# Performance work log

Measured on AMD Instinct MI355X. Metric: run time of the kernel, lower is better.

Reference implementation:

```python
import jax, jax.numpy as jnp
import numpy as np

B, T, D = 4, 2048, 1024
NF = 512
NB = 4
FREQ_SCALE = 0.1


def _w(k, shape, scale):
    return jax.random.normal(k, shape, jnp.float32) * scale


def setup_inputs() -> dict:
    key = jax.random.key(0)
    ks = jax.random.split(key, 16)
    d = D ** -0.5
    inp = {}
    inp['x'] = jax.random.normal(ks[0], (B, T, D), jnp.float32)
    inp['norm_g'] = jnp.ones((D,), jnp.float32)
    inp['norm_b'] = jnp.zeros((D,), jnp.float32)
    inp['Wconcept'] = _w(ks[1], (D, D), d); inp['bconcept'] = jnp.zeros((D,), jnp.float32)
    inp['Wcg'] = _w(ks[2], (D, D), d); inp['bcg'] = jnp.zeros((D,), jnp.float32)
    inp['Wfg'] = _w(ks[3], (NF, D), d); inp['bfg'] = jnp.zeros((NF,), jnp.float32)
    inp['Wtg'] = _w(ks[4], (1, D), d); inp['btg'] = jnp.zeros((1,), jnp.float32)
    inp['Wband'] = _w(ks[5], (NB, D), d); inp['bband'] = jnp.zeros((NB,), jnp.float32)
    inp['Wsp'] = _w(ks[6], (2 * NF, D), d)  # to_spectral, no bias
    inp['freq_importance'] = jnp.ones((NF,), jnp.float32)
    inp['log_decay'] = (jnp.linspace(-3.0, -0.001, NF) + _w(ks[7], (NF,), 0.1)).astype(jnp.float32)
    inp['frequencies'] = ((jnp.arange(NF, dtype=jnp.float32) / NF * 2.0 - 1.0) * 0.2)
    inp['dt'] = jnp.ones((NF,), jnp.float32) * 0.5
    inp['Wgate'] = _w(ks[8], (D, D), d); inp['bgate'] = jnp.zeros((D,), jnp.float32)
    inp['Wfs'] = _w(ks[9], (D, 2 * NF), (2 * NF) ** -0.5)  # from_spectral, no bias
    inp['output_scale'] = jnp.ones((1,), jnp.float32) * 0.5
    inp['norm2_g'] = jnp.ones((D,), jnp.float32)
    inp['norm2_b'] = jnp.zeros((D,), jnp.float32)
    inp['W1'] = _w(ks[10], (4 * D, D), d); inp['b1'] = jnp.zeros((4 * D,), jnp.float32)
    inp['W2'] = _w(ks[11], (D, 4 * D), (4 * D) ** -0.5); inp['b2'] = jnp.zeros((D,), jnp.float32)
    return inp


def _ln(x, g, b):
    m = jnp.mean(x, axis=-1, keepdims=True)
    v = jnp.var(x, axis=-1, keepdims=True)
    return (x - m) * jax.lax.rsqrt(v + 1e-5) * g + b


def reference(x, norm_g, norm_b, Wconcept, bconcept, Wcg, bcg, Wfg, bfg, Wtg, btg,
              Wband, bband, Wsp, freq_importance, log_decay, frequencies, dt,
              Wgate, bgate, Wfs, output_scale, norm2_g, norm2_b, W1, b1, W2, b2):
    b_, t_, _ = x.shape
    nf = log_decay.shape[0]
    nb = Wband.shape[0]
    residual = x
    xn = _ln(x, norm_g, norm_b)

    concept = xn @ Wconcept.T + bconcept
    concept_preserved = concept * jax.nn.sigmoid(xn @ Wcg.T + bcg)

    forget_gates = jax.nn.sigmoid(xn @ Wfg.T + bfg)          # (B,T,NF)
    temporal_strength = jax.nn.sigmoid(xn @ Wtg.T + btg)     # (B,T,1)
    band_strengths = jax.nn.sigmoid(xn @ Wband.T + bband)    # (B,T,NB)

    sp = xn @ Wsp.T                                          # (B,T,2*NF)
    u = jax.lax.complex(sp[..., :nf], sp[..., nf:]) * forget_gates

    decay = jax.nn.sigmoid(log_decay) * (jax.nn.softmax(freq_importance) * nf)
    omega = frequencies * FREQ_SCALE * (jax.nn.sigmoid(dt) * 2.0)
    rot = jax.lax.complex(jnp.cos(omega), jnp.sin(omega))    # (NF,)
    A = decay * rot                                          # (NF,) complex

    band_scale = jnp.repeat(band_strengths, nf // nb, axis=-1)  # (B,T,NF)
    A_exp = A * band_scale                                   # (B,T,NF) complex

    ones_first = jnp.ones((b_, 1, nf), A_exp.dtype)
    powers = jnp.cumprod(jnp.concatenate([ones_first, A_exp[:, :-1, :]], axis=1), axis=1)
    powers = powers * temporal_strength
    kernel = powers * rot

    n_fft = 2 * t_
    Uf = jnp.fft.fft(u, n=n_fft, axis=1)
    Kf = jnp.fft.fft(kernel, n=n_fft, axis=1)
    y = jnp.fft.ifft(Uf * Kf, n=n_fft, axis=1)[:, :t_, :]

    spectral_out = jnp.concatenate([y.real, y.imag], axis=-1)
    y_proj = (spectral_out @ Wfs.T) * output_scale
    gate_values = jax.nn.sigmoid(xn @ Wgate.T + bgate)
    y_gated = (y_proj * gate_values + concept_preserved) / 2.0  # dropout: eval mode

    x2 = residual + y_gated
    xn2 = _ln(x2, norm2_g, norm2_b)
    h = jax.nn.gelu(xn2 @ W1.T + b1, approximate=False)
    return x2 + h @ W2.T + b2
```

## Files before the change

### kernel.cpp

```cpp
#include <hip/hip_runtime.h>
#include <hip/hip_bf16.h>
#include <cstdint>
#include <cstddef>

typedef unsigned short u16;
typedef unsigned int u32;
typedef short bf16x8 __attribute__((ext_vector_type(8)));
typedef float f32x4 __attribute__((ext_vector_type(4)));
typedef float f32x2 __attribute__((ext_vector_type(2)));

static constexpr int Bb = 4, Tt = 2048, Dd = 1024, NFf = 512, NBb = 4;
static constexpr int Mm = Bb * Tt;
static constexpr int NZz = 4736;
static constexpr int Lc = 32;

#define DEV __device__ __forceinline__

typedef const __attribute__((address_space(1))) u32* gas_p;
typedef __attribute__((address_space(3))) u32* las_p;

DEV u16 f2bf(float f) {
    uint32_t u = __float_as_uint(f);
    u = (u + 0x7FFF + ((u >> 16) & 1)) >> 16;
    return (u16)u;
}
DEV float bf2f(u16 h) { return __uint_as_float(((uint32_t)h) << 16); }
DEV float sigm(float x) { return 1.0f / (1.0f + __expf(-x)); }
DEV float gelu_ex(float t) { return 0.5f * t * (1.0f + erff(t * 0.70710678118f)); }

static constexpr int NW0 = NZz * Dd;
static constexpr int NW1 = Dd * 2 * NFf;
static constexpr int NW2 = 4 * Dd * Dd;
static constexpr int NW3 = 4 * Dd * Dd;
static constexpr int NWTOT = NW0 + NW1 + NW2 + NW3;
static constexpr int NWB = NWTOT / 256;

__global__ __launch_bounds__(256) void prep_all(
    const float* __restrict__ Wconcept, const float* __restrict__ Wcg,
    const float* __restrict__ Wfg, const float* __restrict__ Wgate,
    const float* __restrict__ Wsp, const float* __restrict__ Wtg,
    const float* __restrict__ Wband,
    const float* __restrict__ bconcept, const float* __restrict__ bcg,
    const float* __restrict__ bfg, const float* __restrict__ bgate,
    const float* __restrict__ btg, const float* __restrict__ bband,
    const float* __restrict__ Wfs, const float* __restrict__ W1,
    const float* __restrict__ W2,
    const float* __restrict__ fi, const float* __restrict__ logd,
    const float* __restrict__ freqs, const float* __restrict__ dtv,
    const float* __restrict__ x, const float* __restrict__ norm_g,
    const float* __restrict__ norm_b,
    u16* __restrict__ wcat, float* __restrict__ bias_cat,
    u16* __restrict__ wfs, u16* __restrict__ w1b, u16* __restrict__ w2b,
    float* __restrict__ rr, float* __restrict__ ri,
    float* __restrict__ Ar, float* __restrict__ Ai,
    u16* __restrict__ xn)
{
    const int bx = blockIdx.x;
    if (bx == 0) {
        __shared__ float red[256];
        int t = threadIdx.x;
        float v0 = fi[t], v1 = fi[t + 256];
        red[t] = fmaxf(v0, v1); __syncthreads();
        for (int s = 128; s; s >>= 1) { if (t < s) red[t] = fmaxf(red[t], red[t + s]); __syncthreads(); }
        float mx = red[0]; __syncthreads();
        float e0 = expf(v0 - mx), e1 = expf(v1 - mx);
        red[t] = e0 + e1; __syncthreads();
        for (int s = 128; s; s >>= 1) { if (t < s) red[t] += red[t + s]; __syncthreads(); }
        float inv = 1.0f / red[0];
#pragma unroll
        for (int k = 0; k < 2; k++) {
            int f = t + k * 256;
            float e = k ? e1 : e0;
            float decay = sigm(logd[f]) * (e * inv * (float)NFf);
            float omega = freqs[f] * 0.1f * (sigm(dtv[f]) * 2.0f);
            float cc = cosf(omega), ss = sinf(omega);
            rr[f] = cc; ri[f] = ss; Ar[f] = decay * cc; Ai[f] = decay * ss;
        }
        return;
    }
    if (bx <= NWB) {
        int i = (bx - 1) * 256 + threadIdx.x;
        if (i < NW0) {
            int r = i >> 10, c = i & 1023;
            float v;
            if      (r < 1024) v = Wconcept[r * 1024 + c];
            else if (r < 2048) v = Wcg[(r - 1024) * 1024 + c];
            else if (r < 2560) v = Wfg[(r - 2048) * 1024 + c];
            else if (r < 3584) v = Wgate[(r - 2560) * 1024 + c];
            else if (r < 4608) v = Wsp[(r - 3584) * 1024 + c];
            else if (r == 4608) v = Wtg[c];
            else if (r < 4613) v = Wband[(r - 4609) * 1024 + c];
            else v = 0.0f;
            wcat[i] = f2bf(v);
            if (c == 0) {
                float bv;
                if      (r < 1024) bv = bconcept[r];
                else if (r < 2048) bv = bcg[r - 1024];
                else if (r < 2560) bv = bfg[r - 2048];
                else if (r < 3584) bv = bgate[r - 2560];
                else if (r < 4608) bv = 0.0f;
                else if (r == 4608) bv = btg[0];
                else if (r < 4613) bv = bband[r - 4609];
                else bv = 0.0f;
                bias_cat[r] = bv;
            }
        } else if (i < NW0 + NW1) {
            int j = i - NW0; wfs[j] = f2bf(Wfs[j]);
        } else if (i < NW0 + NW1 + NW2) {
            int j = i - NW0 - NW1; w1b[j] = f2bf(W1[j]);
        } else {
            int j = i - NW0 - NW1 - NW2; w2b[j] = f2bf(W2[j]);
        }
        return;
    }
    const int m = bx - NWB - 1, tid = threadIdx.x;
    float4 v = ((const float4*)(x + (size_t)m * Dd))[tid];
    float s1 = v.x + v.y + v.z + v.w;
    float s2 = v.x * v.x + v.y * v.y + v.z * v.z + v.w * v.w;
    __shared__ float lds[16];
    for (int o = 32; o; o >>= 1) { s1 += __shfl_down(s1, o); s2 += __shfl_down(s2, o); }
    int lane = tid & 63, w = tid >> 6;
    if (!lane) { lds[w] = s1; lds[8 + w] = s2; }
    __syncthreads();
    s1 = lds[0] + lds[1] + lds[2] + lds[3];
    s2 = lds[8] + lds[9] + lds[10] + lds[11];
    float mean = s1 * (1.0f / Dd);
    float var  = s2 * (1.0f / Dd) - mean * mean;
    float rstd = rsqrtf(var + 1e-5f);
    float4 gv = ((const float4*)norm_g)[tid];
    float4 bv = ((const float4*)norm_b)[tid];
    ushort4 o;
    o.x = f2bf((v.x - mean) * rstd * gv.x + bv.x);
    o.y = f2bf((v.y - mean) * rstd * gv.y + bv.y);
    o.z = f2bf((v.z - mean) * rstd * gv.z + bv.z);
    o.w = f2bf((v.w - mean) * rstd * gv.w + bv.w);
    ((ushort4*)(xn + (size_t)m * Dd))[tid] = o;
}

template<int MODE>
__global__ __launch_bounds__(256, 3) void gemm_bt(
    const u16* __restrict__ A, const u16* __restrict__ Bw,
    const float* __restrict__ bias, const u16* __restrict__ addb,
    void* __restrict__ Cout, int M, int N, int K)
{
    __shared__ __align__(16) u16 smA[128 * 64];
    __shared__ __align__(16) u16 smB[128 * 64];
    const int tid = threadIdx.x;
    const int m0 = blockIdx.x * 128;
    const int n0 = blockIdx.y * 128;
    const int w = tid >> 6, lane = tid & 63;
    const int wr = w >> 1, wc = w & 1;
    const int quad = lane >> 4, l16 = lane & 15;

    const int r0 = tid >> 3;
    const int cs = (tid & 7) ^ (r0 & 7);
    const u16* gA = A + (size_t)(m0 + r0) * K + cs * 8;
    const u16* gB = Bw + (size_t)(n0 + r0) * K + cs * 8;

    const int swzf = l16 & 7;

    f32x4 acc[4][4];
#pragma unroll
    for (int i = 0; i < 4; i++)
#pragma unroll
        for (int j = 0; j < 4; j++) acc[i][j] = {0.f, 0.f, 0.f, 0.f};

    for (int k0 = 0; k0 < K; k0 += 64) {
        __syncthreads();
#pragma unroll
        for (int j = 0; j < 4; j++) {
            __builtin_amdgcn_global_load_lds((gas_p)(gA + k0 + (size_t)(j * 32) * K),
                                             (las_p)(smA + j * 2048 + tid * 8), 16, 0, 0);
            __builtin_amdgcn_global_load_lds((gas_p)(gB + k0 + (size_t)(j * 32) * K),
                                             (las_p)(smB + j * 2048 + tid * 8), 16, 0, 0);
        }
        __syncthreads();
#pragma unroll
        for (int seg = 0; seg < 2; seg++) {
            bf16x8 af[4], bfv[4];
#pragma unroll
            for (int mi = 0; mi < 4; mi++)
                af[mi] = *(const bf16x8*)&smA[(wr * 64 + mi * 16 + l16) * 64 +
                                              (((seg * 4 + quad) ^ swzf) * 8)];
#pragma unroll
            for (int ni = 0; ni < 4; ni++)
                bfv[ni] = *(const bf16x8*)&smB[(wc * 64 + ni * 16 + l16) * 64 +
                                               (((seg * 4 + quad) ^ swzf) * 8)];
#pragma unroll
            for (int mi = 0; mi < 4; mi++)
#pragma unroll
                for (int ni = 0; ni < 4; ni++)
                    acc[mi][ni] = __builtin_amdgcn_mfma_f32_16x16x32_bf16(
                        af[mi], bfv[ni], acc[mi][ni], 0, 0, 0);
        }
    }

#pragma unroll
    for (int mi = 0; mi < 4; mi++) {
#pragma unroll
        for (int ni = 0; ni < 4; ni++) {
            const int gn = n0 + wc * 64 + ni * 16 + l16;
            const int gm0 = m0 + wr * 64 + mi * 16 + quad * 4;
            if constexpr (MODE == 0 || MODE == 2 || MODE == 4) {
                float bv = (MODE == 4) ? 0.0f : bias[gn];
                float t0 = acc[mi][ni][0] + bv, t1 = acc[mi][ni][1] + bv;
                float t2 = acc[mi][ni][2] + bv, t3 = acc[mi][ni][3] + bv;
                if constexpr (MODE == 2) {
                    t0 = gelu_ex(t0); t1 = gelu_ex(t1); t2 = gelu_ex(t2); t3 = gelu_ex(t3);
                }
                __hip_bfloat162 h01 = __float22bfloat162_rn(float2{t0, t1});
                __hip_bfloat162 h23 = __float22bfloat162_rn(float2{t2, t3});
                __hip_bfloat16* o = (__hip_bfloat16*)Cout;
                o[(size_t)(gm0 + 0) * N + gn] = h01.x;
                o[(size_t)(gm0 + 1) * N + gn] = h01.y;
                o[(size_t)(gm0 + 2) * N + gn] = h23.x;
                o[(size_t)(gm0 + 3) * N + gn] = h23.y;
            } else {
#pragma unroll
                for (int r = 0; r < 4; r++) {
                    const int gm = gm0 + r;
                    ((float*)Cout)[(size_t)gm * N + gn] =
                        acc[mi][ni][r] + bias[gn] + bf2f(addb[(size_t)gm * N + gn]);
                }
            }
        }
    }
}

static constexpr int NBLK_A = (Mm * NFf) / 256;

__global__ __launch_bounds__(256) void prepAk_kernel(
    const u16* __restrict__ Z, ushort2* __restrict__ u2b,
    const float* __restrict__ Ar, const float* __restrict__ Ai,
    const float* __restrict__ rr, const float* __restrict__ ri,
    f32x2* __restrict__ k2)
{
    const int bx = blockIdx.x;
    if (bx < NBLK_A) {
        int i = bx * 256 + threadIdx.x;
        int m = i >> 9, f = i & (NFf - 1);
        const u16* zr = Z + (size_t)m * NZz;
        float fg  = sigm(bf2f(zr[2048 + f]));
        float spr = bf2f(zr[3584 + f]);
        float spi = bf2f(zr[3584 + NFf + f]);
        u2b[i] = ushort2{f2bf(spr * fg), f2bf(spi * fg)};
        return;
    }
    int g = (bx - NBLK_A) * 256 + threadIdx.x;
    int b = g >> 9, f = g & (NFf - 1);
    float Pr = 1.0f, Pi = 0.0f;
    float ar = Ar[f], ai = Ai[f], cr = rr[f], ci = ri[f];
    const int band = f >> 7;
    const u16* zb = Z + (size_t)(b * Tt) * NZz;
    for (int tau = 0; tau < Lc; tau++) {
        const u16* zrow = zb + (size_t)tau * NZz;
        float tsv = sigm(bf2f(zrow[4608]));
        k2[((size_t)b * Lc + tau) * NFf + f] = f32x2{tsv * (cr * Pr - ci * Pi),
                                                     tsv * (cr * Pi + ci * Pr)};
        float bsv = sigm(bf2f(zrow[4609 + band]));
        float er = ar * bsv, ei = ai * bsv;
        float nPr = Pr * er - Pi * ei;
        float nPi = Pr * ei + Pi * er;
        Pr = nPr; Pi = nPi;
    }
}

__global__ __launch_bounds__(256) void conv_kernel(
    const ushort2* __restrict__ u2b, const f32x2* __restrict__ k2,
    u16* __restrict__ spec)
{
    __shared__ f32x2 su[96 * 64];
    __shared__ f32x2 sk[Lc * 64];
    const int tid = threadIdx.x;
    const int fl = tid & 63;
    const int ty = tid >> 6;
    const int f0 = blockIdx.x * 64;
    const int t0 = blockIdx.y * 64;
    const int b  = blockIdx.z;

    for (int i = tid; i < Lc * 64; i += 256) {
        int tau = i >> 6, ff = i & 63;
        sk[i] = k2[((size_t)b * Lc + tau) * NFf + f0 + ff];
    }
    for (int i = tid; i < 96 * 64; i += 256) {
        int r = i >> 6, ff = i & 63;
        int t = t0 - 32 + r;
        f32x2 v = {0.f, 0.f};
        if (t >= 0) {
            ushort2 h = u2b[((size_t)b * Tt + t) * NFf + f0 + ff];
            v = f32x2{bf2f(h.x), bf2f(h.y)};
        }
        su[i] = v;
    }
    __syncthreads();

    const int tl0 = 32 + ty * 16;
    f32x2 win[16], y[16];
#pragma unroll
    for (int j = 0; j < 16; j++) {
        win[j] = su[(tl0 + j) * 64 + fl];
        y[j] = f32x2{0.f, 0.f};
    }
#pragma unroll
    for (int tau = 0; tau < Lc; tau++) {
        f32x2 k = sk[tau * 64 + fl];
#pragma unroll
        for (int j = 0; j < 16; j++) {
            y[j].x += win[j].x * k.x - win[j].y * k.y;
            y[j].y += win[j].x * k.y + win[j].y * k.x;
        }
#pragma unroll
        for (int j = 15; j >= 1; j--) win[j] = win[j - 1];
        win[0] = su[(tl0 - tau - 1) * 64 + fl];
    }
#pragma unroll
    for (int j = 0; j < 16; j++) {
        size_t row = (size_t)(b * Tt + t0 + ty * 16 + j);
        spec[row * (2 * NFf) + f0 + fl]       = f2bf(y[j].x);
        spec[row * (2 * NFf) + NFf + f0 + fl] = f2bf(y[j].y);
    }
}

__global__ __launch_bounds__(256) void fuse2_ln_kernel(
    const float* __restrict__ x, const u16* __restrict__ Z,
    const u16* __restrict__ P2, const float* __restrict__ osc,
    const float* __restrict__ g2, const float* __restrict__ b2v,
    u16* __restrict__ x2b, u16* __restrict__ xn2)
{
    const int m = blockIdx.x, tid = threadIdx.x;
    const float os = osc[0];
    const u16* zr = Z + (size_t)m * NZz;
    float4 xv = ((const float4*)(x + (size_t)m * Dd))[tid];
    ushort4 pv = ((const ushort4*)(P2 + (size_t)m * Dd))[tid];
    float vals[4]; float s1 = 0.0f, s2 = 0.0f;
#pragma unroll
    for (int j = 0; j < 4; j++) {
        int d = tid * 4 + j;
        float concept = bf2f(zr[d]);
        float cg   = sigm(bf2f(zr[1024 + d]));
        float gate = sigm(bf2f(zr[2560 + d]));
        float p = bf2f((&pv.x)[j]);
        float v = (&xv.x)[j] + 0.5f * (p * os * gate + concept * cg);
        vals[j] = v; s1 += v; s2 += v * v;
    }
    __shared__ float lds[16];
    for (int o = 32; o; o >>= 1) { s1 += __shfl_down(s1, o); s2 += __shfl_down(s2, o); }
    int lane = tid & 63, w = tid >> 6;
    if (!lane) { lds[w] = s1; lds[8 + w] = s2; }
    __syncthreads();
    s1 = lds[0] + lds[1] + lds[2] + lds[3];
    s2 = lds[8] + lds[9] + lds[10] + lds[11];
    float mean = s1 * (1.0f / Dd);
    float var  = s2 * (1.0f / Dd) - mean * mean;
    float rstd = rsqrtf(var + 1e-5f);
    ushort4 xo, no;
#pragma unroll
    for (int j = 0; j < 4; j++) {
        int d = tid * 4 + j;
        (&xo.x)[j] = f2bf(vals[j]);
        (&no.x)[j] = f2bf((vals[j] - mean) * rstd * g2[d] + b2v[d]);
    }
    ((ushort4*)(x2b + (size_t)m * Dd))[tid] = xo;
    ((ushort4*)(xn2 + (size_t)m * Dd))[tid] = no;
}

extern "C" void kernel_launch(void* const* d_in, const int* in_sizes, int n_in,
                              void* d_out, int out_size, void* d_ws, size_t ws_size,
                              hipStream_t stream)
{
    const float* x        = (const float*)d_in[0];
    const float* norm_g   = (const float*)d_in[1];
    const float* norm_b   = (const float*)d_in[2];
    const float* Wconcept = (const float*)d_in[3];
    const float* bconcept = (const float*)d_in[4];
    const float* Wcg      = (const float*)d_in[5];
    const float* bcg      = (const float*)d_in[6];
    const float* Wfg      = (const float*)d_in[7];
    const float* bfg      = (const float*)d_in[8];
    const float* Wtg      = (const float*)d_in[9];
    const float* btg      = (const float*)d_in[10];
    const float* Wband    = (const float*)d_in[11];
    const float* bband    = (const float*)d_in[12];
    const float* Wsp      = (const float*)d_in[13];
    const float* fi       = (const float*)d_in[14];
    const float* logd     = (const float*)d_in[15];
    const float* freqs    = (const float*)d_in[16];
    const float* dtv      = (const float*)d_in[17];
    const float* Wgate    = (const float*)d_in[18];
    const float* bgate    = (const float*)d_in[19];
    const float* Wfs      = (const float*)d_in[20];
    const float* osc      = (const float*)d_in[21];
    const float* n2g      = (const float*)d_in[22];
    const float* n2b      = (const float*)d_in[23];
    const float* W1       = (const float*)d_in[24];
    const float* b1       = (const float*)d_in[25];
    const float* W2       = (const float*)d_in[26];
    const float* b2       = (const float*)d_in[27];

    char* ws = (char*)d_ws;
    size_t off = 0;
    auto alloc = [&](size_t bytes) { size_t c = off; off += (bytes + 255) & ~(size_t)255; return c; };
    size_t o_wcat = alloc((size_t)NZz * Dd * 2);
    size_t o_bias = alloc((size_t)NZz * 4);
    size_t o_wfs  = alloc((size_t)Dd * 2 * NFf * 2);
    size_t o_w1   = alloc((size_t)4 * Dd * Dd * 2);
    size_t o_w2   = alloc((size_t)4 * Dd * Dd * 2);
    size_t o_xn   = alloc((size_t)Mm * Dd * 2);
    size_t o_Z    = alloc((size_t)Mm * NZz * 2);
    size_t o_u    = alloc((size_t)Mm * NFf * 4);
    size_t o_spec = alloc((size_t)Mm * Dd * 2);
    size_t o_P2   = alloc((size_t)Mm * Dd * 2);
    size_t o_k2   = alloc((size_t)Bb * Lc * NFf * 8);
    size_t o_rr   = alloc(NFf * 4);
    size_t o_ri   = alloc(NFf * 4);
    size_t o_Ar   = alloc(NFf * 4);
    size_t o_Ai   = alloc(NFf * 4);
    if (ws_size < off) return;

    u16*    wcat = (u16*)(ws + o_wcat);
    float*  bias = (float*)(ws + o_bias);
    u16*    wfs  = (u16*)(ws + o_wfs);
    u16*    w1b  = (u16*)(ws + o_w1);
    u16*    w2b  = (u16*)(ws + o_w2);
    u16*    xn   = (u16*)(ws + o_xn);
    u16*    Zb   = (u16*)(ws + o_Z);
    u16*    hb   = (u16*)(ws + o_Z);
    ushort2* u2b = (ushort2*)(ws + o_u);
    u16*    x2b  = (u16*)(ws + o_u);
    u16*    spec = (u16*)(ws + o_spec);
    u16*    xn2  = (u16*)(ws + o_spec);
    u16*    P2   = (u16*)(ws + o_P2);
    f32x2*  k2   = (f32x2*)(ws + o_k2);
    float*  rr   = (float*)(ws + o_rr);
    float*  ri   = (float*)(ws + o_ri);
    float*  Ar   = (float*)(ws + o_Ar);
    float*  Ai   = (float*)(ws + o_Ai);

    prep_all<<<1 + NWB + Mm, 256, 0, stream>>>(
        Wconcept, Wcg, Wfg, Wgate, Wsp, Wtg, Wband,
        bconcept, bcg, bfg, bgate, btg, bband,
        Wfs, W1, W2, fi, logd, freqs, dtv,
        x, norm_g, norm_b,
        wcat, bias, wfs, w1b, w2b, rr, ri, Ar, Ai, xn);

    gemm_bt<0><<<dim3(Mm / 128, NZz / 128), 256, 0, stream>>>(
        xn, wcat, bias, nullptr, (void*)Zb, Mm, NZz, Dd);

    prepAk_kernel<<<NBLK_A + (Bb * NFf) / 256, 256, 0, stream>>>(
        Zb, u2b, Ar, Ai, rr, ri, k2);

    conv_kernel<<<dim3(NFf / 64, Tt / 64, Bb), 256, 0, stream>>>(u2b, k2, spec);

    gemm_bt<4><<<dim3(Mm / 128, Dd / 128), 256, 0, stream>>>(
        spec, wfs, nullptr, nullptr, (void*)P2, Mm, Dd, 2 * NFf);

    fuse2_ln_kernel<<<Mm, 256, 0, stream>>>(x, Zb, P2, osc, n2g, n2b, x2b, xn2);

    gemm_bt<2><<<dim3(Mm / 128, (4 * Dd) / 128), 256, 0, stream>>>(
        xn2, w1b, b1, nullptr, (void*)hb, Mm, 4 * Dd, Dd);
    gemm_bt<3><<<dim3(Mm / 128, Dd / 128), 256, 0, stream>>>(
        hb, w2b, b2, x2b, d_out, Mm, Dd, 4 * Dd);
}
```

Before: 528.2 us.

## Add 256x256 ping-pong MFMA GEMM for input projection and FFN up-projection

Adds a new 512-thread GEMM kernel with 256x256 output tiles, double-buffered direct global-to-LDS loads, and interleaved quadrant MFMA phases using barriers and s_setprio. It replaces the 128x128 GEMM for the large concatenated projection and for the W1+GELU layer. NZz is padded from 4736 to 4864 so it divides by 256. The larger tiles aim to raise arithmetic intensity and overlap loads with MFMA work, at the cost of extra padded columns, more registers and LDS, and fewer blocks per CU.

```diff
diff --git a/kernel.cpp b/kernel.cpp
--- a/kernel.cpp
+++ b/kernel.cpp
@@ -11,7 +11,7 @@
 
 static constexpr int Bb = 4, Tt = 2048, Dd = 1024, NFf = 512, NBb = 4;
 static constexpr int Mm = Bb * Tt;
-static constexpr int NZz = 4736;
+static constexpr int NZz = 4864;
 static constexpr int Lc = 32;
 
 #define DEV __device__ __forceinline__
@@ -201,13 +201,9 @@
         for (int ni = 0; ni < 4; ni++) {
             const int gn = n0 + wc * 64 + ni * 16 + l16;
             const int gm0 = m0 + wr * 64 + mi * 16 + quad * 4;
-            if constexpr (MODE == 0 || MODE == 2 || MODE == 4) {
-                float bv = (MODE == 4) ? 0.0f : bias[gn];
-                float t0 = acc[mi][ni][0] + bv, t1 = acc[mi][ni][1] + bv;
-                float t2 = acc[mi][ni][2] + bv, t3 = acc[mi][ni][3] + bv;
-                if constexpr (MODE == 2) {
-                    t0 = gelu_ex(t0); t1 = gelu_ex(t1); t2 = gelu_ex(t2); t3 = gelu_ex(t3);
-                }
+            if constexpr (MODE == 4) {
+                float t0 = acc[mi][ni][0], t1 = acc[mi][ni][1];
+                float t2 = acc[mi][ni][2], t3 = acc[mi][ni][3];
                 __hip_bfloat162 h01 = __float22bfloat162_rn(float2{t0, t1});
                 __hip_bfloat162 h23 = __float22bfloat162_rn(float2{t2, t3});
                 __hip_bfloat16* o = (__hip_bfloat16*)Cout;
@@ -224,6 +220,151 @@
                 }
             }
         }
+    }
+}
+
+template<int MODE>
+__global__ __launch_bounds__(512, 2) void gemm_bt256(
+    const u16* __restrict__ A, const u16* __restrict__ Bw,
+    const float* __restrict__ bias,
+    void* __restrict__ Cout, int M, int N, int K)
+{
+    __shared__ __align__(16) u16 smA[2][256 * 64];
+    __shared__ __align__(16) u16 smB[2][256 * 64];
+    const int tid = threadIdx.x;
+    const int m0 = blockIdx.x * 256;
+    const int n0 = blockIdx.y * 256;
+    const int w = tid >> 6, lane = tid & 63;
+    const int wr = w >> 2, wc = w & 3;
+    const int quad = lane >> 4, l16 = lane & 15;
+    const int swzf = l16 & 7;
+
+    const int rs = tid >> 3;
+    const int cs = (tid & 7) ^ (rs & 7);
+    const u16* gA = A + (size_t)(m0 + rs) * K + cs * 8;
+    const u16* gB = Bw + (size_t)(n0 + rs) * K + cs * 8;
+
+    f32x4 acc[2][2][4][2];
+#pragma unroll
+    for (int qa = 0; qa < 2; qa++)
+#pragma unroll
+        for (int qb = 0; qb < 2; qb++)
+#pragma unroll
+            for (int mi = 0; mi < 4; mi++)
+#pragma unroll
+                for (int ni = 0; ni < 2; ni++) acc[qa][qb][mi][ni] = {0.f, 0.f, 0.f, 0.f};
+
+    bf16x8 af[4][2], bf0[2][2], bf1[2][2];
+
+#define STG_A(BUF, H, KO) do { \
+    __builtin_amdgcn_global_load_lds((gas_p)(gA + (size_t)((H) * 128) * K + (KO)), \
+        (las_p)(&smA[BUF][(H) * 128 * 64 + tid * 8]), 16, 0, 0); \
+    __builtin_amdgcn_global_load_lds((gas_p)(gA + (size_t)((H) * 128 + 64) * K + (KO)), \
+        (las_p)(&smA[BUF][((H) * 128 + 64) * 64 + tid * 8]), 16, 0, 0); \
+} while (0)
+#define STG_B(BUF, H, KO) do { \
+    __builtin_amdgcn_global_load_lds((gas_p)(gB + (size_t)((H) * 128) * K + (KO)), \
+        (las_p)(&smB[BUF][(H) * 128 * 64 + tid * 8]), 16, 0, 0); \
+    __builtin_amdgcn_global_load_lds((gas_p)(gB + (size_t)((H) * 128 + 64) * K + (KO)), \
+        (las_p)(&smB[BUF][((H) * 128 + 64) * 64 + tid * 8]), 16, 0, 0); \
+} while (0)
+#define LOAD_AF(QA) do { \
+    _Pragma("unroll") for (int mi = 0; mi < 4; mi++) \
+    _Pragma("unroll") for (int kk = 0; kk < 2; kk++) \
+        af[mi][kk] = *(const bf16x8*)&smA[cur][((QA) * 128 + wr * 64 + mi * 16 + l16) * 64 + \
+                                              (((kk * 4 + quad) ^ swzf) * 8)]; \
+} while (0)
+#define LOAD_BF(QB, BF) do { \
+    _Pragma("unroll") for (int ni = 0; ni < 2; ni++) \
+    _Pragma("unroll") for (int kk = 0; kk < 2; kk++) \
+        BF[ni][kk] = *(const bf16x8*)&smB[cur][((QB) * 128 + wc * 32 + ni * 16 + l16) * 64 + \
+                                               (((kk * 4 + quad) ^ swzf) * 8)]; \
+} while (0)
+#define MFMA16(QA, QB, BF) do { \
+    _Pragma("unroll") for (int mi = 0; mi < 4; mi++) \
+    _Pragma("unroll") for (int ni = 0; ni < 2; ni++) \
+    _Pragma("unroll") for (int kk = 0; kk < 2; kk++) \
+        acc[QA][QB][mi][ni] = __builtin_amdgcn_mfma_f32_16x16x32_bf16( \
+            af[mi][kk], BF[ni][kk], acc[QA][QB][mi][ni], 0, 0, 0); \
+} while (0)
+
+    const int NT = K >> 6;
+    STG_A(0, 0, 0); STG_A(0, 1, 0);
+    STG_B(0, 0, 0); STG_B(0, 1, 0);
+    STG_A(1, 0, 64); STG_B(1, 0, 64);
+    asm volatile("s_waitcnt vmcnt(4)" ::: "memory");
+    __builtin_amdgcn_s_barrier();
+    asm volatile("" ::: "memory");
+
+    for (int t = 0; t < NT; ++t) {
+        const int cur = t & 1, nxt = cur ^ 1;
+        const int kn1 = (t + 1) << 6, kn2 = (t + 2) << 6;
+        const bool i1 = (t + 1) < NT, i2 = (t + 2) < NT;
+        LOAD_AF(0);
+        LOAD_BF(0, bf0);
+        if (i1) STG_A(nxt, 1, kn1);
+        __builtin_amdgcn_s_barrier();
+        asm volatile("s_waitcnt lgkmcnt(0)" ::: "memory");
+        __builtin_amdgcn_s_setprio(1);
+        MFMA16(0, 0, bf0);
+        __builtin_amdgcn_s_setprio(0);
+        __builtin_amdgcn_s_barrier();
+        LOAD_BF(1, bf1);
+        if (i1) STG_B(nxt, 1, kn1);
+        __builtin_amdgcn_s_barrier();
+        asm volatile("s_waitcnt lgkmcnt(0)" ::: "memory");
+        __builtin_amdgcn_s_setprio(1);
+        MFMA16(0, 1, bf1);
+        __builtin_amdgcn_s_setprio(0);
+        __builtin_amdgcn_s_barrier();
+        LOAD_AF(1);
+        if (i2) STG_A(cur, 0, kn2);
+        __builtin_amdgcn_s_barrier();
+        asm volatile("s_waitcnt lgkmcnt(0)" ::: "memory");
+        __builtin_amdgcn_s_setprio(1);
+        MFMA16(1, 0, bf0);
+        __builtin_amdgcn_s_setprio(0);
+        __builtin_amdgcn_s_barrier();
+        if (i2) STG_B(cur, 0, kn2);
+        __builtin_amdgcn_s_barrier();
+        __builtin_amdgcn_s_setprio(1);
+        MFMA16(1, 1, bf1);
+        __builtin_amdgcn_s_setprio(0);
+        if (i2) asm volatile("s_waitcnt vmcnt(4)" ::: "memory");
+        else    asm volatile("s_waitcnt vmcnt(0)" ::: "memory");
+        __builtin_amdgcn_s_barrier();
+        asm volatile("" ::: "memory");
+    }
+
+#undef STG_A
+#undef STG_B
+#undef LOAD_AF
+#undef LOAD_BF
+#undef MFMA16
+
+#pragma unroll
+    for (int qa = 0; qa < 2; qa++)
+#pragma unroll
+    for (int qb = 0; qb < 2; qb++)
+#pragma unroll
+    for (int mi = 0; mi < 4; mi++)
+#pragma unroll
+    for (int ni = 0; ni < 2; ni++) {
+        const int gn = n0 + qb * 128 + wc * 32 + ni * 16 + l16;
+        const int gm0 = m0 + qa * 128 + wr * 64 + mi * 16 + quad * 4;
+        const float bv = bias[gn];
+        float t0 = acc[qa][qb][mi][ni][0] + bv, t1 = acc[qa][qb][mi][ni][1] + bv;
+        float t2 = acc[qa][qb][mi][ni][2] + bv, t3 = acc[qa][qb][mi][ni][3] + bv;
+        if constexpr (MODE == 2) {
+            t0 = gelu_ex(t0); t1 = gelu_ex(t1); t2 = gelu_ex(t2); t3 = gelu_ex(t3);
+        }
+        __hip_bfloat162 h01 = __float22bfloat162_rn(float2{t0, t1});
+        __hip_bfloat162 h23 = __float22bfloat162_rn(float2{t2, t3});
+        __hip_bfloat16* o = (__hip_bfloat16*)Cout;
+        o[(size_t)(gm0 + 0) * N + gn] = h01.x;
+        o[(size_t)(gm0 + 1) * N + gn] = h01.y;
+        o[(size_t)(gm0 + 2) * N + gn] = h23.x;
+        o[(size_t)(gm0 + 3) * N + gn] = h23.y;
     }
 }
 
@@ -443,8 +584,8 @@
         x, norm_g, norm_b,
         wcat, bias, wfs, w1b, w2b, rr, ri, Ar, Ai, xn);
 
-    gemm_bt<0><<<dim3(Mm / 128, NZz / 128), 256, 0, stream>>>(
-        xn, wcat, bias, nullptr, (void*)Zb, Mm, NZz, Dd);
+    gemm_bt256<0><<<dim3(Mm / 256, NZz / 256), 512, 0, stream>>>(
+        xn, wcat, bias, (void*)Zb, Mm, NZz, Dd);
 
     prepAk_kernel<<<NBLK_A + (Bb * NFf) / 256, 256, 0, stream>>>(
         Zb, u2b, Ar, Ai, rr, ri, k2);
@@ -456,8 +597,8 @@
 
     fuse2_ln_kernel<<<Mm, 256, 0, stream>>>(x, Zb, P2, osc, n2g, n2b, x2b, xn2);
 
-    gemm_bt<2><<<dim3(Mm / 128, (4 * Dd) / 128), 256, 0, stream>>>(
-        xn2, w1b, b1, nullptr, (void*)hb, Mm, 4 * Dd, Dd);
+    gemm_bt256<2><<<dim3(Mm / 256, (4 * Dd) / 256), 512, 0, stream>>>(
+        xn2, w1b, b1, (void*)hb, Mm, 4 * Dd, Dd);
     gemm_bt<3><<<dim3(Mm / 128, Dd / 128), 256, 0, stream>>>(
         hb, w2b, b2, x2b, d_out, Mm, Dd, 4 * Dd);
 }
```

Result: slower. 557.5 us (+5.5%).
